# Kernel tuning notes

Measured on AMD Instinct MI355X. Metric: run time of the kernel, lower is better.

Reference implementation:

```python
import jax, jax.numpy as jnp
import numpy as np

N, P, G = 524288, 16, 8


def setup_inputs() -> dict:
    key = jax.random.key(0)
    k1, k2, k3, k4, k5 = jax.random.split(key, 5)
    # Strictly positive data (Box-Cox transform uses log / fractional powers)
    X = jax.random.uniform(k1, (N, P), dtype=jnp.float32) + 0.1
    # Box-Cox powers away from 0 to avoid division blow-up
    lambdas = jax.random.uniform(k2, (P, 1), dtype=jnp.float32) + 0.5
    # Means near the transformed-data range so densities don't underflow
    mus = 0.1 * jax.random.normal(k3, (G, P), dtype=jnp.float32) - 0.3
    # SPD covariances: 0.25*I + A A^T
    A = 0.05 * jax.random.normal(k4, (G, P, P), dtype=jnp.float32)
    sigmas = 0.25 * jnp.eye(P, dtype=jnp.float32)[None] + jnp.einsum('gpq,grq->gpr', A, A)
    w = jax.random.uniform(k5, (G, 1), dtype=jnp.float32)
    return {"X": X, "lambdas": lambdas, "mus": mus, "sigmas": sigmas, "w": w}


def reference(X, lambdas, mus, sigmas, w):
    # objective_fn of the GMM: negative log-likelihood of a Box-Cox GMM.
    n, p = X.shape
    lam = lambdas[:, 0]                                  # (p,)
    Xt = (X ** lam - 1.0) / lam                          # Box-Cox transform, (n,p)
    Sinv = jnp.linalg.inv(sigmas)                        # (G,p,p), once per component
    logdet = jnp.linalg.slogdet(sigmas)[1]               # (G,)
    d = Xt[:, None, :] - mus[None, :, :]                 # (n,G,p)
    quad = jnp.einsum('ngp,gpq,ngq->ng', d, Sinv, d)     # batched Mahalanobis, (n,G)
    lead = -0.5 * p * jnp.log(jnp.float32(2.0) * jnp.pi)
    jac = jnp.log(X) @ (lam - 1.0)                       # log-Jacobian of Box-Cox, (n,)
    ldens = -0.5 * quad + lead - 0.5 * logdet[None, :] + jac[:, None]  # (n,G)
    W = jax.nn.softmax(w[:, 0])                          # mixing proportions, (G,)
    mixed = (jnp.exp(ldens) * W).sum(-1)                 # (n,)
    return -jnp.log(mixed).sum()
```

## Files before the change

kernel.cpp:

```cpp
#include <hip/hip_runtime.h>
#include <hip/hip_bf16.h>


#define P 16
#define G 8

typedef short bf16x8 __attribute__((ext_vector_type(8)));
typedef float f32x4 __attribute__((ext_vector_type(4)));

__device__ __forceinline__ unsigned short f2bf(float f) {
    union { float f; unsigned u; } c; c.f = f;
    unsigned u = c.u;
    return (unsigned short)((u + 0x7FFFu + ((u >> 16) & 1u)) >> 16);
}

#define WS_LC   2048
#define WS_LAM  2056
#define WS_LM1  2072
#define WS_RL   2088

__global__ __launch_bounds__(128) void gmm_prep(const float* __restrict__ lambdas,
                                                const float* __restrict__ mus,
                                                const float* __restrict__ sigmas,
                                                const float* __restrict__ w,
                                                float* __restrict__ ws,
                                                float* __restrict__ out) {
    __shared__ float Lsh[G][P][P];
    __shared__ float Vsh[G][P][P];
    __shared__ float ldet[G];
    const int tid = threadIdx.x;
    const int g = tid >> 4;
    const int r = tid & 15;

    float Srow[P], Lrow[P];
#pragma unroll
    for (int j = 0; j < P; ++j) Srow[j] = sigmas[g * P * P + r * P + j];

#pragma unroll
    for (int j = 0; j < P; ++j) {
        float s = Srow[j];
#pragma unroll
        for (int k = 0; k < P; ++k) {
            if (k < j) s -= Lrow[k] * Lsh[g][j][k];
        }
        if (r == j) {
            float dv = sqrtf(s);
            Lrow[j] = dv;
            Lsh[g][j][j] = dv;
        }
        __syncthreads();
        if (r > j) {
            float dv = s / Lsh[g][j][j];
            Lrow[j] = dv;
            Lsh[g][r][j] = dv;
        }
        __syncthreads();
    }

    if (r == 0) {
        float ld = 0.f;
#pragma unroll
        for (int j = 0; j < P; ++j) ld += __logf(Lsh[g][j][j]);
        ldet[g] = 2.0f * ld;
    }

    float col[P];
#pragma unroll
    for (int i = 0; i < P; ++i) {
        float s = 0.f;
#pragma unroll
        for (int k = 0; k < P; ++k) {
            if (k < i) s += Lsh[g][i][k] * col[k];
        }
        float rii = 1.0f / Lsh[g][i][i];
        col[i] = (i == r) ? rii : -s * rii;
    }
#pragma unroll
    for (int i = 0; i < P; ++i) Vsh[g][i][r] = col[i];
    __syncthreads();

    float u = 0.f;
#pragma unroll
    for (int j = 0; j < P; ++j) u = fmaf(Vsh[g][r][j], mus[g * P + j], u);

    unsigned short* ws16 = (unsigned short*)ws;
#pragma unroll
    for (int qq = 0; qq < 4; ++qq) {
        const int lane = qq * 16 + r;
#pragma unroll
        for (int j = 0; j < 8; ++j) {
            float val;
            if (qq == 0)      val = Vsh[g][r][j];
            else if (qq == 1) val = Vsh[g][r][8 + j];
            else if (qq == 2) val = (j == 0) ? -u : 0.f;
            else              val = 0.f;
            ws16[(g * 64 + lane) * 8 + j] = f2bf(val);
        }
    }

    if (tid == 0) {
        float wm = w[0];
#pragma unroll
        for (int k = 1; k < G; ++k) wm = fmaxf(wm, w[k]);
        float s = 0.f;
#pragma unroll
        for (int k = 0; k < G; ++k) s += __expf(w[k] - wm);
        const float lse = wm + __logf(s);
        const float lead = -14.7030165f;
#pragma unroll
        for (int k = 0; k < G; ++k)
            ws[WS_LC + k] = (w[k] - lse) + lead - 0.5f * ldet[k];
        out[0] = 0.f;
    }
    if (tid < P) {
        float lam = lambdas[tid];
        ws[WS_LAM + tid] = lam;
        ws[WS_LM1 + tid] = lam - 1.0f;
        ws[WS_RL  + tid] = 1.0f / lam;
    }
}

__global__ __launch_bounds__(256) void gmm_main(const float* __restrict__ X,
                                                const float* __restrict__ ws,
                                                float* __restrict__ out,
                                                int nrows) {
    __shared__ __align__(16) unsigned short sxt[256 * 16];
    __shared__ float red[4];

    const int tid  = threadIdx.x;
    const int lane = tid & 63;
    const int wid  = tid >> 6;
    const int lq   = lane >> 4;
    const int ln15 = lane & 15;
    const unsigned short* ws16 = (const unsigned short*)ws;

    bf16x8 afrag[G];
#pragma unroll
    for (int g = 0; g < G; ++g)
        afrag[g] = *(const bf16x8*)(ws16 + (g * 64 + lane) * 8);

    const int row = blockIdx.x * 256 + tid;
    const int rclamp = row < nrows ? row : nrows - 1;
    const float4* Xv = (const float4*)(X + (size_t)rclamp * P);
    float4 q0 = Xv[0], q1 = Xv[1], q2 = Xv[2], q3 = Xv[3];
    float xv[P] = {q0.x, q0.y, q0.z, q0.w, q1.x, q1.y, q1.z, q1.w,
                   q2.x, q2.y, q2.z, q2.w, q3.x, q3.y, q3.z, q3.w};

    float xt[P];
    float jac = 0.f;
#pragma unroll
    for (int p = 0; p < P; ++p) {
        float ln = __logf(xv[p]);
        xt[p] = (__expf(ws[WS_LAM + p] * ln) - 1.0f) * ws[WS_RL + p];
        jac = fmaf(ln, ws[WS_LM1 + p], jac);
    }

#pragma unroll
    for (int h = 0; h < 2; ++h) {
        union { unsigned u[4]; bf16x8 v; } c;
#pragma unroll
        for (int e = 0; e < 4; ++e)
            c.u[e] = (unsigned)f2bf(xt[h * 8 + e * 2]) |
                     ((unsigned)f2bf(xt[h * 8 + e * 2 + 1]) << 16);
        *(bf16x8*)(sxt + tid * 16 + h * 8) = c.v;
    }
    __syncthreads();

    float qsel[G];
#pragma unroll
    for (int q = 0; q < 4; ++q) {
        bf16x8 bfrag;
        if (lq < 2) {
            bfrag = *(const bf16x8*)(sxt + (wid * 64 + q * 16 + ln15) * 16 + lq * 8);
        } else {
            union { unsigned u[4]; bf16x8 v; } c;
            c.u[0] = (lq == 2) ? 0x3F80u : 0u;
            c.u[1] = 0u; c.u[2] = 0u; c.u[3] = 0u;
            bfrag = c.v;
        }
#pragma unroll
        for (int g = 0; g < G; ++g) {
            f32x4 acc = {0.f, 0.f, 0.f, 0.f};
            acc = __builtin_amdgcn_mfma_f32_16x16x32_bf16(afrag[g], bfrag, acc, 0, 0, 0);
            float partial = acc[0] * acc[0];
            partial = fmaf(acc[1], acc[1], partial);
            partial = fmaf(acc[2], acc[2], partial);
            partial = fmaf(acc[3], acc[3], partial);
            float p1 = partial + __shfl_xor(partial, 16, 64);
            float qf = p1 + __shfl_xor(p1, 32, 64);
            qsel[g] = (lq == q) ? qf : ((q == 0) ? 0.f : qsel[g]);
        }
    }

    float mixed = 0.f;
#pragma unroll
    for (int g = 0; g < G; ++g)
        mixed += __expf(fmaf(-0.5f, qsel[g], ws[WS_LC + g] + jac));

    float nll = (row < nrows) ? -__logf(mixed) : 0.f;

#pragma unroll
    for (int off = 32; off > 0; off >>= 1) nll += __shfl_down(nll, off, 64);
    if (lane == 0) red[wid] = nll;
    __syncthreads();
    if (tid == 0) atomicAdd(out, red[0] + red[1] + red[2] + red[3]);
}

extern "C" void kernel_launch(void* const* d_in, const int* in_sizes, int n_in,
                              void* d_out, int out_size, void* d_ws, size_t ws_size,
                              hipStream_t stream) {
    const float* X       = (const float*)d_in[0];
    const float* lambdas = (const float*)d_in[1];
    const float* mus     = (const float*)d_in[2];
    const float* sigmas  = (const float*)d_in[3];
    const float* w       = (const float*)d_in[4];
    float* out = (float*)d_out;
    float* ws  = (float*)d_ws;

    const int nrows = in_sizes[0] / P;

    gmm_prep<<<1, 128, 0, stream>>>(lambdas, mus, sigmas, w, ws, out);
    gmm_main<<<(nrows + 255) / 256, 256, 0, stream>>>(X, ws, out, nrows);
}
```

Baseline: 113.8 us.

## Replace bf16 MFMA Mahalanobis with per-thread fp32 triangular FMA loop

Drops the bf16 MFMA path, its LDS staging and shuffles for the quadratic form. Each thread now computes the Mahalanobis distance directly in fp32 with the lower-triangular inverse Cholesky factor, which the prep kernel stores as plain floats in the workspace. That removes the LDS round trip, the sync, the bf16 conversion and the wasted MFMA lanes, and restores fp32 precision. The cost is about 8*136 scalar FMAs per row plus many uniform workspace loads, which may make the kernel ALU-bound.

```diff
diff --git a/kernel.cpp b/kernel.cpp
--- a/kernel.cpp
+++ b/kernel.cpp
@@ -5,19 +5,11 @@
 #define P 16
 #define G 8
 
-typedef short bf16x8 __attribute__((ext_vector_type(8)));
-typedef float f32x4 __attribute__((ext_vector_type(4)));
-
-__device__ __forceinline__ unsigned short f2bf(float f) {
-    union { float f; unsigned u; } c; c.f = f;
-    unsigned u = c.u;
-    return (unsigned short)((u + 0x7FFFu + ((u >> 16) & 1u)) >> 16);
-}
-
-#define WS_LC   2048
-#define WS_LAM  2056
-#define WS_LM1  2072
-#define WS_RL   2088
+#define GSTRIDE 272
+#define WS_LC   (G * GSTRIDE)
+#define WS_LAM  (WS_LC + G)
+#define WS_LM1  (WS_LAM + P)
+#define WS_RL   (WS_LM1 + P)
 
 __global__ __launch_bounds__(128) void gmm_prep(const float* __restrict__ lambdas,
                                                 const float* __restrict__ mus,
@@ -76,27 +68,16 @@
         col[i] = (i == r) ? rii : -s * rii;
     }
 #pragma unroll
-    for (int i = 0; i < P; ++i) Vsh[g][i][r] = col[i];
+    for (int i = 0; i < P; ++i) {
+        Vsh[g][i][r] = col[i];
+        ws[g * GSTRIDE + i * P + r] = col[i];
+    }
     __syncthreads();
 
     float u = 0.f;
 #pragma unroll
     for (int j = 0; j < P; ++j) u = fmaf(Vsh[g][r][j], mus[g * P + j], u);
-
-    unsigned short* ws16 = (unsigned short*)ws;
-#pragma unroll
-    for (int qq = 0; qq < 4; ++qq) {
-        const int lane = qq * 16 + r;
-#pragma unroll
-        for (int j = 0; j < 8; ++j) {
-            float val;
-            if (qq == 0)      val = Vsh[g][r][j];
-            else if (qq == 1) val = Vsh[g][r][8 + j];
-            else if (qq == 2) val = (j == 0) ? -u : 0.f;
-            else              val = 0.f;
-            ws16[(g * 64 + lane) * 8 + j] = f2bf(val);
-        }
-    }
+    ws[g * GSTRIDE + 256 + r] = u;
 
     if (tid == 0) {
         float wm = w[0];
@@ -124,20 +105,11 @@
                                                 const float* __restrict__ ws,
                                                 float* __restrict__ out,
                                                 int nrows) {
-    __shared__ __align__(16) unsigned short sxt[256 * 16];
     __shared__ float red[4];
 
     const int tid  = threadIdx.x;
     const int lane = tid & 63;
     const int wid  = tid >> 6;
-    const int lq   = lane >> 4;
-    const int ln15 = lane & 15;
-    const unsigned short* ws16 = (const unsigned short*)ws;
-
-    bf16x8 afrag[G];
-#pragma unroll
-    for (int g = 0; g < G; ++g)
-        afrag[g] = *(const bf16x8*)(ws16 + (g * 64 + lane) * 8);
 
     const int row = blockIdx.x * 256 + tid;
     const int rclamp = row < nrows ? row : nrows - 1;
@@ -155,47 +127,21 @@
         jac = fmaf(ln, ws[WS_LM1 + p], jac);
     }
 
-#pragma unroll
-    for (int h = 0; h < 2; ++h) {
-        union { unsigned u[4]; bf16x8 v; } c;
-#pragma unroll
-        for (int e = 0; e < 4; ++e)
-            c.u[e] = (unsigned)f2bf(xt[h * 8 + e * 2]) |
-                     ((unsigned)f2bf(xt[h * 8 + e * 2 + 1]) << 16);
-        *(bf16x8*)(sxt + tid * 16 + h * 8) = c.v;
-    }
-    __syncthreads();
-
-    float qsel[G];
-#pragma unroll
-    for (int q = 0; q < 4; ++q) {
-        bf16x8 bfrag;
-        if (lq < 2) {
-            bfrag = *(const bf16x8*)(sxt + (wid * 64 + q * 16 + ln15) * 16 + lq * 8);
-        } else {
-            union { unsigned u[4]; bf16x8 v; } c;
-            c.u[0] = (lq == 2) ? 0x3F80u : 0u;
-            c.u[1] = 0u; c.u[2] = 0u; c.u[3] = 0u;
-            bfrag = c.v;
-        }
-#pragma unroll
-        for (int g = 0; g < G; ++g) {
-            f32x4 acc = {0.f, 0.f, 0.f, 0.f};
-            acc = __builtin_amdgcn_mfma_f32_16x16x32_bf16(afrag[g], bfrag, acc, 0, 0, 0);
-            float partial = acc[0] * acc[0];
-            partial = fmaf(acc[1], acc[1], partial);
-            partial = fmaf(acc[2], acc[2], partial);
-            partial = fmaf(acc[3], acc[3], partial);
-            float p1 = partial + __shfl_xor(partial, 16, 64);
-            float qf = p1 + __shfl_xor(p1, 32, 64);
-            qsel[g] = (lq == q) ? qf : ((q == 0) ? 0.f : qsel[g]);
-        }
-    }
-
     float mixed = 0.f;
 #pragma unroll
-    for (int g = 0; g < G; ++g)
-        mixed += __expf(fmaf(-0.5f, qsel[g], ws[WS_LC + g] + jac));
+    for (int g = 0; g < G; ++g) {
+        const float* __restrict__ Vg = ws + g * GSTRIDE;
+        float quad = 0.f;
+#pragma unroll
+        for (int i = 0; i < P; ++i) {
+            float y = -Vg[256 + i];
+#pragma unroll
+            for (int j = 0; j <= i; ++j)
+                y = fmaf(Vg[i * P + j], xt[j], y);
+            quad = fmaf(y, y, quad);
+        }
+        mixed += __expf(fmaf(-0.5f, quad, ws[WS_LC + g] + jac));
+    }
 
     float nll = (row < nrows) ? -__logf(mixed) : 0.f;
 
```

After: 128.7 us. 13.0% more time.
